# Kernel tuning notes

Hardware: AMD Instinct MI355X
Metric: run time of the kernel (lower is better)

Reference implementation:

```python
import jax, jax.numpy as jnp
import numpy as np

N_NODES = 50000
N_EDGES = 640000
IN_C, HID_C, OUT_C = 64, 128, 64


def _glorot(key, fan_in, fan_out):
    lim = float(np.sqrt(6.0 / (fan_in + fan_out)))
    return jax.random.uniform(key, (fan_in, fan_out), jnp.float32, -lim, lim)


def setup_inputs() -> dict:
    key = jax.random.key(0)
    ks = jax.random.split(key, 16)
    x = jax.random.normal(ks[0], (N_NODES, IN_C), jnp.float32)
    edge_index = jax.random.randint(ks[1], (2, N_EDGES), 0, N_NODES, jnp.int64)
    # SAGEConv params: out = mean_aggr(x_j) @ Wl + x @ Wr + b
    dims = [(IN_C, HID_C), (HID_C, HID_C), (HID_C, OUT_C)]
    params = {}
    for i, (fi, fo) in enumerate(dims):
        params[f"Wl{i}"] = _glorot(ks[2 + 3 * i], fi, fo)
        params[f"Wr{i}"] = _glorot(ks[3 + 3 * i], fi, fo)
        params[f"b{i}"] = jnp.zeros((fo,), jnp.float32)
    # classifier: Linear(64,32) -> ReLU -> Linear(32,1) -> Sigmoid (dropout off in eval)
    params["Wc1"] = _glorot(ks[11], OUT_C, 32)
    params["bc1"] = jnp.zeros((32,), jnp.float32)
    params["Wc2"] = _glorot(ks[12], 32, 1)
    params["bc2"] = jnp.zeros((1,), jnp.float32)
    return {"x": x, "edge_index": edge_index, **params}


def _sage_conv(x, src, dst, Wl, Wr, b):
    # gather neighbor (source) features along edges, mean-aggregate at target
    msgs = x[src]                                                    # [E, C]
    agg = jax.ops.segment_sum(msgs, dst, num_segments=N_NODES)      # [N, C]
    deg = jax.ops.segment_sum(jnp.ones((src.shape[0], 1), x.dtype), dst,
                              num_segments=N_NODES)                 # [N, 1]
    agg = agg / jnp.maximum(deg, 1.0)
    return agg @ Wl + x @ Wr + b


def reference(x, edge_index, Wl0, Wr0, b0, Wl1, Wr1, b1, Wl2, Wr2, b2,
              Wc1, bc1, Wc2, bc2):
    src, dst = edge_index[0], edge_index[1]
    h = jax.nn.relu(_sage_conv(x, src, dst, Wl0, Wr0, b0))
    h = jax.nn.relu(_sage_conv(h, src, dst, Wl1, Wr1, b1))
    h = _sage_conv(h, src, dst, Wl2, Wr2, b2)                       # [N, 64]
    h = jax.nn.relu(h @ Wc1 + bc1)                                  # [N, 32]
    return jax.nn.sigmoid(h @ Wc2 + bc2)                            # [N, 1]
```

## Files before the change

### kernel.cpp

```cpp
#include <hip/hip_runtime.h>
#include <hip/hip_cooperative_groups.h>
#include <math.h>

namespace cg = cooperative_groups;

#define NN 50000
#define NE 640000
#define CAP 64

typedef short short8 __attribute__((ext_vector_type(8)));
typedef float f32x4  __attribute__((ext_vector_type(4)));

__device__ __forceinline__ unsigned bfr(float f) {
    unsigned u = __float_as_uint(f);
    return (u + 0x7FFFu + ((u >> 16) & 1u)) >> 16;
}
__device__ __forceinline__ unsigned pk2(float a, float b) { return bfr(a) | (bfr(b) << 16); }
__device__ __forceinline__ float bflo(unsigned u) { return __uint_as_float(u << 16); }
__device__ __forceinline__ float bfhi(unsigned u) { return __uint_as_float(u & 0xFFFF0000u); }

__device__ __forceinline__ void packOne(const float* Wl, const float* Wr,
                                        unsigned short* wp, int idx,
                                        int CIN, int COUT) {
    int k = idx / COUT, n = idx % COUT;
    float v = (k < CIN) ? Wl[k * COUT + n] : Wr[(k - CIN) * COUT + n];
    int kt = k >> 5, quad = (k >> 3) & 3, j = k & 7;
    int nt = n >> 4, l16 = n & 15;
    int NT = COUT / 16;
    wp[(((kt * NT + nt) * 64) + quad * 16 + l16) * 8 + j] = (unsigned short)bfr(v);
}

template <int CIN, int COUT, bool RELU, bool CLS>
__device__ __forceinline__ void
fused_layer(const unsigned* __restrict__ Fu, const unsigned short* __restrict__ Fs,
            const int* __restrict__ nbr, const int* __restrict__ cnt,
            const unsigned short* __restrict__ Wpack, const float* __restrict__ bias,
            unsigned short* __restrict__ outp,
            const unsigned short* __restrict__ WpackC, const float* __restrict__ bc1,
            const float* __restrict__ Wc2, const float* __restrict__ bc2,
            float* __restrict__ outf,
            short* __restrict__ lds, int blk, int gstride, int t) {
    constexpr int RU = CIN / 2;
    constexpr int PC = RU / 16;
    constexpr int RS = CIN + 8;
    constexpr int RSu = RS / 2;
    constexpr int KT = (2 * CIN) / 32;
    constexpr int NT = COUT / 16;
    constexpr int CS = 136;
    const int NTILE = (NN + 127) / 128;

    const int g = t >> 4, lg = t & 15;
    const int wave = t >> 6, lane = t & 63;
    const int quad = lane >> 4, l16 = lane & 15;

    for (int tile = blk; tile < NTILE; tile += gstride) {
#pragma unroll 1
        for (int i = 0; i < 8; ++i) {
            const int rloc = g * 8 + i;
            const int gw = tile * 128 + rloc;
            unsigned* lrow = (unsigned*)lds + rloc * RSu + lg * PC;
            if (gw < NN) {
                const int deg = cnt[gw];
                const int m = (deg < CAP) ? deg : CAP;
                float a[2 * PC] = {};
                for (int base = 0; base < m; base += 16) {
                    int idx = NN;
                    if (base + lg < m) idx = nbr[gw * CAP + base + lg];
#pragma unroll
                    for (int j = 0; j < 16; ++j) {
                        const int n = __shfl(idx, j, 16);
                        if (PC == 2) {
                            const uint2 u = *(const uint2*)(Fu + (size_t)n * RU + lg * 2);
                            a[0] += bflo(u.x); a[1] += bfhi(u.x);
                            a[2] += bflo(u.y); a[3] += bfhi(u.y);
                        } else {
                            const uint4 u = *(const uint4*)(Fu + (size_t)n * RU + lg * 4);
                            a[0] += bflo(u.x); a[1] += bfhi(u.x);
                            a[2] += bflo(u.y); a[3] += bfhi(u.y);
                            a[4] += bflo(u.z); a[5] += bfhi(u.z);
                            a[6] += bflo(u.w); a[7] += bfhi(u.w);
                        }
                    }
                }
                const float di = 1.0f / (float)((deg > 1) ? deg : 1);
                if (PC == 2)
                    *(uint2*)lrow = make_uint2(pk2(a[0] * di, a[1] * di),
                                               pk2(a[2] * di, a[3] * di));
                else
                    *(uint4*)lrow = make_uint4(pk2(a[0] * di, a[1] * di),
                                               pk2(a[2] * di, a[3] * di),
                                               pk2(a[4] * di, a[5] * di),
                                               pk2(a[6] * di, a[7] * di));
            } else {
                if (PC == 2) *(uint2*)lrow = make_uint2(0u, 0u);
                else         *(uint4*)lrow = make_uint4(0u, 0u, 0u, 0u);
            }
        }
        __syncthreads();

        const int rbase = tile * 128 + wave * 32;
        int r0 = rbase + l16;      if (r0 >= NN) r0 = NN - 1;
        int r1 = rbase + 16 + l16; if (r1 >= NN) r1 = NN - 1;
        const int rl0 = wave * 32 + l16, rl1 = rl0 + 16;

        f32x4 acc[2][NT] = {};
#pragma unroll
        for (int kt = 0; kt < KT; ++kt) {
            short8 a0, a1;
            if (kt < KT / 2) {
                a0 = *(const short8*)(lds + rl0 * RS + kt * 32 + quad * 8);
                a1 = *(const short8*)(lds + rl1 * RS + kt * 32 + quad * 8);
            } else {
                a0 = *(const short8*)(Fs + (size_t)r0 * CIN + (kt * 32 - CIN) + quad * 8);
                a1 = *(const short8*)(Fs + (size_t)r1 * CIN + (kt * 32 - CIN) + quad * 8);
            }
#pragma unroll
            for (int nt = 0; nt < NT; ++nt) {
                const short8 bfrag = *(const short8*)(Wpack + (size_t)((kt * NT + nt) * 64 + lane) * 8);
                acc[0][nt] = __builtin_amdgcn_mfma_f32_16x16x32_bf16(a0, bfrag, acc[0][nt], 0, 0, 0);
                acc[1][nt] = __builtin_amdgcn_mfma_f32_16x16x32_bf16(a1, bfrag, acc[1][nt], 0, 0, 0);
            }
        }
        __syncthreads();

        if constexpr (!CLS) {
#pragma unroll
            for (int nt = 0; nt < NT; ++nt) {
                const float bb = bias[nt * 16 + l16];
#pragma unroll
                for (int s = 0; s < 2; ++s)
#pragma unroll
                    for (int rg = 0; rg < 4; ++rg) {
                        const int rloc = wave * 32 + s * 16 + quad * 4 + rg;
                        float v = acc[s][nt][rg] + bb;
                        if (RELU) v = fmaxf(v, 0.f);
                        lds[rloc * CS + nt * 16 + l16] = (short)(unsigned short)bfr(v);
                    }
            }
            __syncthreads();
            constexpr int CH = COUT / 8;
            for (int idx = t; idx < 128 * CH; idx += 256) {
                const int row = idx / CH, c8 = idx % CH;
                const int gr = tile * 128 + row;
                if (gr < NN)
                    *(uint4*)(outp + (size_t)gr * COUT + c8 * 8) =
                        *(const uint4*)(lds + row * CS + c8 * 8);
            }
            __syncthreads();
        } else {
            constexpr int HS = 72;
#pragma unroll
            for (int nt = 0; nt < NT; ++nt) {
                const float bb = bias[nt * 16 + l16];
#pragma unroll
                for (int s = 0; s < 2; ++s)
#pragma unroll
                    for (int rg = 0; rg < 4; ++rg) {
                        const int rloc = wave * 32 + s * 16 + quad * 4 + rg;
                        lds[rloc * HS + nt * 16 + l16] =
                            (short)(unsigned short)bfr(acc[s][nt][rg] + bb);
                    }
            }
            __syncthreads();

            f32x4 sacc[2][2] = {};
#pragma unroll
            for (int s = 0; s < 2; ++s) {
                const int rloc = wave * 32 + s * 16 + l16;
#pragma unroll
                for (int kt2 = 0; kt2 < 2; ++kt2) {
                    const short8 af = *(const short8*)(lds + rloc * HS + kt2 * 32 + quad * 8);
#pragma unroll
                    for (int nt2 = 0; nt2 < 2; ++nt2) {
                        const short8 bf = *(const short8*)(WpackC + (size_t)((kt2 * 2 + nt2) * 64 + lane) * 8);
                        sacc[s][nt2] = __builtin_amdgcn_mfma_f32_16x16x32_bf16(af, bf, sacc[s][nt2], 0, 0, 0);
                    }
                }
            }

            const float b1a = bc1[l16], b1b = bc1[16 + l16];
            const float w2a = Wc2[l16], w2b = Wc2[16 + l16];
            const float b2v = bc2[0];
#pragma unroll
            for (int s = 0; s < 2; ++s)
#pragma unroll
                for (int rg = 0; rg < 4; ++rg) {
                    float p = fmaxf(sacc[s][0][rg] + b1a, 0.f) * w2a +
                              fmaxf(sacc[s][1][rg] + b1b, 0.f) * w2b;
#pragma unroll
                    for (int off = 1; off < 16; off <<= 1) p += __shfl_xor(p, off);
                    if (l16 == 0) {
                        const int row = tile * 128 + wave * 32 + s * 16 + quad * 4 + rg;
                        if (row < NN) outf[row] = 1.0f / (1.0f + expf(-(p + b2v)));
                    }
                }
            __syncthreads();
        }
    }
}

__global__ __launch_bounds__(256) void
k_all(const int* __restrict__ src, const int* __restrict__ dst,
      const float* __restrict__ x,
      const float* Wl0, const float* Wr0, const float* b0,
      const float* Wl1, const float* Wr1, const float* b1,
      const float* Wl2, const float* Wr2, const float* b2,
      const float* Wc1, const float* bc1, const float* Wc2, const float* bc2,
      int* cnt, int* nbr, unsigned short* xb,
      unsigned short* wp0, unsigned short* wp1, unsigned short* wp2,
      unsigned short* wpc,
      unsigned short* aggb, unsigned short* h0b, unsigned short* h1b,
      float* out) {
    cg::grid_group grid = cg::this_grid();
    (void)aggb;

    __shared__ __align__(16) short lds[128 * 136];

    const int t = threadIdx.x, b = blockIdx.x;
    const int nthr = gridDim.x * 256;
    const int gt = b * 256 + t;

    for (int e = gt; e < NE; e += nthr) {
        int d = dst[e];
        int p = atomicAdd(&cnt[d], 1);
        if (p < CAP) nbr[d * CAP + p] = src[e];
    }
    for (int i = gt; i < NN * 16; i += nthr) {
        float4 v = ((const float4*)x)[i];
        ((uint2*)xb)[i] = make_uint2(pk2(v.x, v.y), pk2(v.z, v.w));
    }
    if (gt < 32) ((unsigned*)xb)[(size_t)NN * 32 + gt] = 0u;
    else if (gt < 96) ((unsigned*)h0b)[(size_t)NN * 64 + (gt - 32)] = 0u;
    else if (gt < 160) ((unsigned*)h1b)[(size_t)NN * 64 + (gt - 96)] = 0u;
    for (int i = gt; i < 67584; i += nthr) {
        if (i < 16384) packOne(Wl0, Wr0, wp0, i, 64, 128);
        else if (i < 49152) packOne(Wl1, Wr1, wp1, i - 16384, 128, 128);
        else if (i < 65536) packOne(Wl2, Wr2, wp2, i - 49152, 128, 64);
        else packOne(Wc1, Wc1, wpc, i - 65536, 64, 32);
    }
    grid.sync();

    fused_layer<64, 128, true, false>((const unsigned*)xb, xb, nbr, cnt, wp0, b0, h0b,
                                      nullptr, nullptr, nullptr, nullptr, nullptr,
                                      lds, b, gridDim.x, t);
    grid.sync();

    fused_layer<128, 128, true, false>((const unsigned*)h0b, h0b, nbr, cnt, wp1, b1, h1b,
                                       nullptr, nullptr, nullptr, nullptr, nullptr,
                                       lds, b, gridDim.x, t);
    grid.sync();

    fused_layer<128, 64, false, true>((const unsigned*)h1b, h1b, nbr, cnt, wp2, b2, nullptr,
                                      wpc, bc1, Wc2, bc2, out,
                                      lds, b, gridDim.x, t);
}

template <int LOGC>
__device__ __forceinline__ void
agg_phase(const unsigned* __restrict__ xu, const int* __restrict__ nbr,
          const int* __restrict__ cnt, unsigned* __restrict__ aggu,
          int gid, int ngroups, int l16) {
    constexpr int RU = 1 << (LOGC - 1);
    constexpr int PC = RU / 16;

    for (int gw = gid; gw < NN; gw += ngroups) {
        const int deg = cnt[gw];
        const int m = (deg < CAP) ? deg : CAP;

        float a[2 * PC] = {};

        for (int base = 0; base < m; base += 16) {
            int idx = NN;
            if (base + l16 < m) idx = nbr[gw * CAP + base + l16];
#pragma unroll
            for (int j = 0; j < 16; ++j) {
                const int n = __shfl(idx, j, 16);
                if (PC == 2) {
                    const uint2 u = *(const uint2*)(xu + (size_t)n * RU + l16 * 2);
                    a[0] += bflo(u.x); a[1] += bfhi(u.x);
                    a[2] += bflo(u.y); a[3] += bfhi(u.y);
                } else {
                    const uint4 u = *(const uint4*)(xu + (size_t)n * RU + l16 * 4);
                    a[0] += bflo(u.x); a[1] += bfhi(u.x);
                    a[2] += bflo(u.y); a[3] += bfhi(u.y);
                    a[4] += bflo(u.z); a[5] += bfhi(u.z);
                    a[6] += bflo(u.w); a[7] += bfhi(u.w);
                }
            }
        }

        const float di = 1.0f / (float)((deg > 1) ? deg : 1);
        if (PC == 2) {
            uint2 o = make_uint2(pk2(a[0] * di, a[1] * di), pk2(a[2] * di, a[3] * di));
            *(uint2*)(aggu + (size_t)gw * RU + l16 * 2) = o;
        } else {
            uint4 o = make_uint4(pk2(a[0] * di, a[1] * di), pk2(a[2] * di, a[3] * di),
                                 pk2(a[4] * di, a[5] * di), pk2(a[6] * di, a[7] * di));
            *(uint4*)(aggu + (size_t)gw * RU + l16 * 4) = o;
        }
    }
}

template <int CIN, int COUT, bool RELU>
__device__ __forceinline__ void
mfma_phase(const unsigned short* __restrict__ Agg, const unsigned short* __restrict__ X,
           const unsigned short* __restrict__ Wpack, const float* __restrict__ bias,
           unsigned short* __restrict__ outp, int blk, int gstride, int wave, int lane) {
    constexpr int KT = (2 * CIN) / 32;
    constexpr int NT = COUT / 16;
    const int quad = lane >> 4, l16 = lane & 15;
    const int NTILE = (NN + 127) / 128;

    for (int tile = blk; tile < NTILE; tile += gstride) {
        const int row_base = tile * 128 + wave * 32;
        int r0 = row_base + l16;      if (r0 >= NN) r0 = NN - 1;
        int r1 = row_base + 16 + l16; if (r1 >= NN) r1 = NN - 1;

        f32x4 acc[2][NT] = {};

        for (int kt = 0; kt < KT; ++kt) {
            const unsigned short* P = (kt < KT / 2) ? Agg : X;
            const int kb = (kt < KT / 2) ? kt * 32 : kt * 32 - CIN;
            const short8 a0 = *(const short8*)(P + (size_t)r0 * CIN + kb + quad * 8);
            const short8 a1 = *(const short8*)(P + (size_t)r1 * CIN + kb + quad * 8);
#pragma unroll
            for (int nt = 0; nt < NT; ++nt) {
                const short8 bfrag = *(const short8*)(Wpack + (size_t)((kt * NT + nt) * 64 + lane) * 8);
                acc[0][nt] = __builtin_amdgcn_mfma_f32_16x16x32_bf16(a0, bfrag, acc[0][nt], 0, 0, 0);
                acc[1][nt] = __builtin_amdgcn_mfma_f32_16x16x32_bf16(a1, bfrag, acc[1][nt], 0, 0, 0);
            }
        }

#pragma unroll
        for (int nt = 0; nt < NT; ++nt) {
            const int col = nt * 16 + l16;
            const float bb = bias[col];
#pragma unroll
            for (int s = 0; s < 2; ++s) {
#pragma unroll
                for (int rg = 0; rg < 4; ++rg) {
                    int row = row_base + s * 16 + quad * 4 + rg;
                    if (row < NN) {
                        float v = acc[s][nt][rg] + bb;
                        if (RELU) v = fmaxf(v, 0.f);
                        outp[(size_t)row * COUT + col] = (unsigned short)bfr(v);
                    }
                }
            }
        }
    }
}

__global__ __launch_bounds__(256) void
k_prep(const int* __restrict__ src, const int* __restrict__ dst,
       int* __restrict__ cnt, int* __restrict__ nbr,
       const float* __restrict__ x, unsigned* __restrict__ xb,
       const float* Wl0, const float* Wr0, const float* Wl1, const float* Wr1,
       const float* Wl2, const float* Wr2, const float* Wc1,
       unsigned short* wp0, unsigned short* wp1, unsigned short* wp2,
       unsigned short* wpc, unsigned short* h0b, unsigned short* h1b) {
    const int b = blockIdx.x, t = threadIdx.x;
    if (b < 2500) {
        int e = b * 256 + t;
        if (e < NE) {
            int d = dst[e];
            int p = atomicAdd(&cnt[d], 1);
            if (p < CAP) nbr[d * CAP + p] = src[e];
        }
        if (b == 0) {
            if (t < 32) xb[(size_t)NN * 32 + t] = 0u;
            else if (t < 96) ((unsigned*)h0b)[(size_t)NN * 64 + (t - 32)] = 0u;
            else if (t < 160) ((unsigned*)h1b)[(size_t)NN * 64 + (t - 96)] = 0u;
        }
    } else if (b < 5625) {
        int i = (b - 2500) * 256 + t;
        if (i < NN * 16) {
            float4 v = ((const float4*)x)[i];
            ((uint2*)xb)[i] = make_uint2(pk2(v.x, v.y), pk2(v.z, v.w));
        }
    } else {
        int idx = (b - 5625) * 256 + t;
        if (idx < 16384) packOne(Wl0, Wr0, wp0, idx, 64, 128);
        else if (idx < 49152) packOne(Wl1, Wr1, wp1, idx - 16384, 128, 128);
        else if (idx < 65536) packOne(Wl2, Wr2, wp2, idx - 49152, 128, 64);
        else if (idx < 67584) packOne(Wc1, Wc1, wpc, idx - 65536, 64, 32);
    }
}

template <int LOGC>
__global__ __launch_bounds__(256) void
k_aggregate(const unsigned* __restrict__ xu, const int* __restrict__ nbr,
            const int* __restrict__ cnt, unsigned* __restrict__ aggu, int N) {
    const int gid = (blockIdx.x * 256 + threadIdx.x) >> 4;
    if (gid >= N) return;
    agg_phase<LOGC>(xu, nbr, cnt, aggu, gid, 1 << 30, threadIdx.x & 15);
}

template <int CIN, int COUT, bool RELU>
__global__ __launch_bounds__(256) void
k_mfma(const unsigned short* __restrict__ Agg, const unsigned short* __restrict__ X,
       const unsigned short* __restrict__ Wpack, const float* __restrict__ bias,
       unsigned short* __restrict__ outp, int N) {
    mfma_phase<CIN, COUT, RELU>(Agg, X, Wpack, bias, outp,
                                blockIdx.x, 1 << 30, threadIdx.x >> 6, threadIdx.x & 63);
}

__global__ __launch_bounds__(256) void
k_mfma_cls(const unsigned short* __restrict__ Agg, const unsigned short* __restrict__ X,
           const unsigned short* __restrict__ Wpack, const unsigned short* __restrict__ WpackC,
           const float* __restrict__ bias, const float* __restrict__ bc1,
           const float* __restrict__ Wc2, const float* __restrict__ bc2,
           float* __restrict__ out, int N) {
    constexpr int CIN = 128, NT = 4, KT = 8;

    __shared__ __align__(16) short Hs[8 * 16 * 64];

    const int t = threadIdx.x;
    const int wave = t >> 6, lane = t & 63;
    const int quad = lane >> 4, l16 = lane & 15;

    const int row_base = blockIdx.x * 128 + wave * 32;
    int r0 = row_base + l16;      if (r0 >= N) r0 = N - 1;
    int r1 = row_base + 16 + l16; if (r1 >= N) r1 = N - 1;

    f32x4 acc[2][NT] = {};

    for (int kt = 0; kt < KT; ++kt) {
        const unsigned short* P = (kt < KT / 2) ? Agg : X;
        const int kb = (kt < KT / 2) ? kt * 32 : kt * 32 - CIN;
        const short8 a0 = *(const short8*)(P + (size_t)r0 * CIN + kb + quad * 8);
        const short8 a1 = *(const short8*)(P + (size_t)r1 * CIN + kb + quad * 8);
#pragma unroll
        for (int nt = 0; nt < NT; ++nt) {
            const short8 bfrag = *(const short8*)(Wpack + (size_t)((kt * NT + nt) * 64 + lane) * 8);
            acc[0][nt] = __builtin_amdgcn_mfma_f32_16x16x32_bf16(a0, bfrag, acc[0][nt], 0, 0, 0);
            acc[1][nt] = __builtin_amdgcn_mfma_f32_16x16x32_bf16(a1, bfrag, acc[1][nt], 0, 0, 0);
        }
    }

#pragma unroll
    for (int nt = 0; nt < NT; ++nt) {
        const float bb = bias[nt * 16 + l16];
#pragma unroll
        for (int s = 0; s < 2; ++s)
#pragma unroll
            for (int rg = 0; rg < 4; ++rg)
                Hs[(wave * 2 + s) * 1024 + (quad * 4 + rg) * 64 + nt * 16 + l16] =
                    (unsigned short)bfr(acc[s][nt][rg] + bb);
    }
    __syncthreads();

    f32x4 sacc[2][2] = {};
#pragma unroll
    for (int s = 0; s < 2; ++s)
#pragma unroll
        for (int kt2 = 0; kt2 < 2; ++kt2) {
            const short8 af = *(const short8*)&Hs[(wave * 2 + s) * 1024 + l16 * 64 +
                                                  kt2 * 32 + quad * 8];
#pragma unroll
            for (int nt2 = 0; nt2 < 2; ++nt2) {
                const short8 bf = *(const short8*)(WpackC + (size_t)((kt2 * 2 + nt2) * 64 + lane) * 8);
                sacc[s][nt2] = __builtin_amdgcn_mfma_f32_16x16x32_bf16(af, bf, sacc[s][nt2], 0, 0, 0);
            }
        }

    const float b1a = bc1[l16], b1b = bc1[16 + l16];
    const float w2a = Wc2[l16], w2b = Wc2[16 + l16];
    const float b2v = bc2[0];
#pragma unroll
    for (int s = 0; s < 2; ++s)
#pragma unroll
        for (int rg = 0; rg < 4; ++rg) {
            float p = fmaxf(sacc[s][0][rg] + b1a, 0.f) * w2a +
                      fmaxf(sacc[s][1][rg] + b1b, 0.f) * w2b;
#pragma unroll
            for (int off = 1; off < 16; off <<= 1) p += __shfl_xor(p, off);
            if (l16 == 0) {
                int row = row_base + s * 16 + quad * 4 + rg;
                if (row < N) out[row] = 1.0f / (1.0f + expf(-(p + b2v)));
            }
        }
}

extern "C" void kernel_launch(void* const* d_in, const int* in_sizes, int n_in,
                              void* d_out, int out_size, void* d_ws, size_t ws_size,
                              hipStream_t stream) {
    const float* x   = (const float*)d_in[0];
    const int*   ei  = (const int*)d_in[1];
    const int*   src = ei;
    const int*   dst = ei + NE;
    const float* Wl0 = (const float*)d_in[2];
    const float* Wr0 = (const float*)d_in[3];
    const float* b0  = (const float*)d_in[4];
    const float* Wl1 = (const float*)d_in[5];
    const float* Wr1 = (const float*)d_in[6];
    const float* b1  = (const float*)d_in[7];
    const float* Wl2 = (const float*)d_in[8];
    const float* Wr2 = (const float*)d_in[9];
    const float* b2  = (const float*)d_in[10];
    const float* Wc1 = (const float*)d_in[11];
    const float* bc1 = (const float*)d_in[12];
    const float* Wc2 = (const float*)d_in[13];
    const float* bc2 = (const float*)d_in[14];
    float* out = (float*)d_out;

    char*  ws   = (char*)d_ws;
    int*   cnt  = (int*)(ws);
    unsigned short* wp0 = (unsigned short*)(ws + (size_t)256 * 1024);
    unsigned short* wp1 = (unsigned short*)(ws + (size_t)352 * 1024);
    unsigned short* wp2 = (unsigned short*)(ws + (size_t)448 * 1024);
    unsigned short* wpc = (unsigned short*)(ws + (size_t)512 * 1024);
    int*   nbr  = (int*)(ws + (size_t)1 * (1 << 20));
    unsigned short* xb   = (unsigned short*)(ws + (size_t)16 * (1 << 20));
    unsigned short* aggb = (unsigned short*)(ws + (size_t)24 * (1 << 20));
    unsigned short* h0b  = (unsigned short*)(ws + (size_t)40 * (1 << 20));
    unsigned short* h1b  = (unsigned short*)(ws + (size_t)56 * (1 << 20));

    hipMemsetAsync(cnt, 0, (size_t)NN * sizeof(int), stream);

    bool coop_ok = false;
    int maxBpc = 0, ncu = 0, dev = 0;
    hipGetDevice(&dev);
    hipDeviceGetAttribute(&ncu, hipDeviceAttributeMultiprocessorCount, dev);
    hipError_t qerr = hipOccupancyMaxActiveBlocksPerMultiprocessor(
        &maxBpc, (const void*)k_all, 256, 0);
    if (qerr == hipSuccess && maxBpc > 0 && ncu > 0) {
        int grid = maxBpc * ncu;
        if (grid > 2048) grid = 2048;
        const int* srcp = src; const int* dstp = dst;
        void* args[] = {
            (void*)&srcp, (void*)&dstp, (void*)&x,
            (void*)&Wl0, (void*)&Wr0, (void*)&b0,
            (void*)&Wl1, (void*)&Wr1, (void*)&b1,
            (void*)&Wl2, (void*)&Wr2, (void*)&b2,
            (void*)&Wc1, (void*)&bc1, (void*)&Wc2, (void*)&bc2,
            (void*)&cnt, (void*)&nbr, (void*)&xb,
            (void*)&wp0, (void*)&wp1, (void*)&wp2, (void*)&wpc,
            (void*)&aggb, (void*)&h0b, (void*)&h1b,
            (void*)&out
        };
        hipError_t lerr = hipLaunchCooperativeKernel((const void*)k_all, dim3(grid),
                                                     dim3(256), args, 0, stream);
        if (lerr == hipSuccess) coop_ok = true;
        else (void)hipGetLastError();
    } else {
        (void)hipGetLastError();
    }

    if (!coop_ok) {
        const int B = 256;
        const int AGG_GRID = (NN * 16 + 255) / 256;
        const int MFMA_GRID = (NN + 127) / 128;

        k_prep<<<5889, B, 0, stream>>>(src, dst, cnt, nbr, x, (unsigned*)xb,
                                       Wl0, Wr0, Wl1, Wr1, Wl2, Wr2, Wc1,
                                       wp0, wp1, wp2, wpc, h0b, h1b);

        k_aggregate<6><<<AGG_GRID, B, 0, stream>>>((const unsigned*)xb, nbr, cnt,
                                                   (unsigned*)aggb, NN);
        k_mfma<64, 128, true><<<MFMA_GRID, B, 0, stream>>>(aggb, xb, wp0, b0, h0b, NN);

        k_aggregate<7><<<AGG_GRID, B, 0, stream>>>((const unsigned*)h0b, nbr, cnt,
                                                   (unsigned*)aggb, NN);
        k_mfma<128, 128, true><<<MFMA_GRID, B, 0, stream>>>(aggb, h0b, wp1, b1, h1b, NN);

        k_aggregate<7><<<AGG_GRID, B, 0, stream>>>((const unsigned*)h1b, nbr, cnt,
                                                   (unsigned*)aggb, NN);
        k_mfma_cls<<<MFMA_GRID, B, 0, stream>>>(aggb, h1b, wp2, wpc, b2, bc1, Wc2, bc2,
                                                out, NN);
    }
}
```

Measured before the change: 234.3 us.

## Replace cooperative persistent kernel with per-layer fused kernel launches

Drops the single cooperative kernel that used grid-wide syncs between phases. It is replaced by a prep kernel followed by three launches, one per layer, each fusing aggregation with the MFMA matmul and using one block per 128-row tile. Kernel boundaries now provide the inter-layer synchronization, and grid occupancy is no longer capped by the resident-block limit. The cost is extra launch overhead and less flexible load balancing across tiles.

```diff
diff --git a/kernel.cpp b/kernel.cpp
--- a/kernel.cpp
+++ b/kernel.cpp
@@ -1,8 +1,5 @@
 #include <hip/hip_runtime.h>
-#include <hip/hip_cooperative_groups.h>
 #include <math.h>
-
-namespace cg = cooperative_groups;
 
 #define NN 50000
 #define NE 640000
@@ -39,7 +36,7 @@
             const unsigned short* __restrict__ WpackC, const float* __restrict__ bc1,
             const float* __restrict__ Wc2, const float* __restrict__ bc2,
             float* __restrict__ outf,
-            short* __restrict__ lds, int blk, int gstride, int t) {
+            short* __restrict__ lds, int tile, int t) {
     constexpr int RU = CIN / 2;
     constexpr int PC = RU / 16;
     constexpr int RS = CIN + 8;
@@ -47,308 +44,166 @@
     constexpr int KT = (2 * CIN) / 32;
     constexpr int NT = COUT / 16;
     constexpr int CS = 136;
-    const int NTILE = (NN + 127) / 128;
 
     const int g = t >> 4, lg = t & 15;
     const int wave = t >> 6, lane = t & 63;
     const int quad = lane >> 4, l16 = lane & 15;
 
-    for (int tile = blk; tile < NTILE; tile += gstride) {
 #pragma unroll 1
-        for (int i = 0; i < 8; ++i) {
-            const int rloc = g * 8 + i;
-            const int gw = tile * 128 + rloc;
-            unsigned* lrow = (unsigned*)lds + rloc * RSu + lg * PC;
-            if (gw < NN) {
-                const int deg = cnt[gw];
-                const int m = (deg < CAP) ? deg : CAP;
-                float a[2 * PC] = {};
-                for (int base = 0; base < m; base += 16) {
-                    int idx = NN;
-                    if (base + lg < m) idx = nbr[gw * CAP + base + lg];
-#pragma unroll
-                    for (int j = 0; j < 16; ++j) {
-                        const int n = __shfl(idx, j, 16);
-                        if (PC == 2) {
-                            const uint2 u = *(const uint2*)(Fu + (size_t)n * RU + lg * 2);
-                            a[0] += bflo(u.x); a[1] += bfhi(u.x);
-                            a[2] += bflo(u.y); a[3] += bfhi(u.y);
-                        } else {
-                            const uint4 u = *(const uint4*)(Fu + (size_t)n * RU + lg * 4);
-                            a[0] += bflo(u.x); a[1] += bfhi(u.x);
-                            a[2] += bflo(u.y); a[3] += bfhi(u.y);
-                            a[4] += bflo(u.z); a[5] += bfhi(u.z);
-                            a[6] += bflo(u.w); a[7] += bfhi(u.w);
-                        }
+    for (int i = 0; i < 8; ++i) {
+        const int rloc = g * 8 + i;
+        const int gw = tile * 128 + rloc;
+        unsigned* lrow = (unsigned*)lds + rloc * RSu + lg * PC;
+        if (gw < NN) {
+            const int deg = cnt[gw];
+            const int m = (deg < CAP) ? deg : CAP;
+            float a[2 * PC] = {};
+            for (int base = 0; base < m; base += 16) {
+                int idx = NN;
+                if (base + lg < m) idx = nbr[gw * CAP + base + lg];
+#pragma unroll
+                for (int j = 0; j < 16; ++j) {
+                    const int n = __shfl(idx, j, 16);
+                    if (PC == 2) {
+                        const uint2 u = *(const uint2*)(Fu + (size_t)n * RU + lg * 2);
+                        a[0] += bflo(u.x); a[1] += bfhi(u.x);
+                        a[2] += bflo(u.y); a[3] += bfhi(u.y);
+                    } else {
+                        const uint4 u = *(const uint4*)(Fu + (size_t)n * RU + lg * 4);
+                        a[0] += bflo(u.x); a[1] += bfhi(u.x);
+                        a[2] += bflo(u.y); a[3] += bfhi(u.y);
+                        a[4] += bflo(u.z); a[5] += bfhi(u.z);
+                        a[6] += bflo(u.w); a[7] += bfhi(u.w);
                     }
                 }
-                const float di = 1.0f / (float)((deg > 1) ? deg : 1);
-                if (PC == 2)
-                    *(uint2*)lrow = make_uint2(pk2(a[0] * di, a[1] * di),
-                                               pk2(a[2] * di, a[3] * di));
-                else
-                    *(uint4*)lrow = make_uint4(pk2(a[0] * di, a[1] * di),
-                                               pk2(a[2] * di, a[3] * di),
-                                               pk2(a[4] * di, a[5] * di),
-                                               pk2(a[6] * di, a[7] * di));
-            } else {
-                if (PC == 2) *(uint2*)lrow = make_uint2(0u, 0u);
-                else         *(uint4*)lrow = make_uint4(0u, 0u, 0u, 0u);
             }
+            const float di = 1.0f / (float)((deg > 1) ? deg : 1);
+            if (PC == 2)
+                *(uint2*)lrow = make_uint2(pk2(a[0] * di, a[1] * di),
+                                           pk2(a[2] * di, a[3] * di));
+            else
+                *(uint4*)lrow = make_uint4(pk2(a[0] * di, a[1] * di),
+                                           pk2(a[2] * di, a[3] * di),
+                                           pk2(a[4] * di, a[5] * di),
+                                           pk2(a[6] * di, a[7] * di));
+        } else {
+            if (PC == 2) *(uint2*)lrow = make_uint2(0u, 0u);
+            else         *(uint4*)lrow = make_uint4(0u, 0u, 0u, 0u);
+        }
+    }
+    __syncthreads();
+
+    const int rbase = tile * 128 + wave * 32;
+    int r0 = rbase + l16;      if (r0 >= NN) r0 = NN - 1;
+    int r1 = rbase + 16 + l16; if (r1 >= NN) r1 = NN - 1;
+    const int rl0 = wave * 32 + l16, rl1 = rl0 + 16;
+
+    f32x4 acc[2][NT] = {};
+#pragma unroll
+    for (int kt = 0; kt < KT; ++kt) {
+        short8 a0, a1;
+        if (kt < KT / 2) {
+            a0 = *(const short8*)(lds + rl0 * RS + kt * 32 + quad * 8);
+            a1 = *(const short8*)(lds + rl1 * RS + kt * 32 + quad * 8);
+        } else {
+            a0 = *(const short8*)(Fs + (size_t)r0 * CIN + (kt * 32 - CIN) + quad * 8);
+            a1 = *(const short8*)(Fs + (size_t)r1 * CIN + (kt * 32 - CIN) + quad * 8);
+        }
+#pragma unroll
+        for (int nt = 0; nt < NT; ++nt) {
+            const short8 bfrag = *(const short8*)(Wpack + (size_t)((kt * NT + nt) * 64 + lane) * 8);
+            acc[0][nt] = __builtin_amdgcn_mfma_f32_16x16x32_bf16(a0, bfrag, acc[0][nt], 0, 0, 0);
+            acc[1][nt] = __builtin_amdgcn_mfma_f32_16x16x32_bf16(a1, bfrag, acc[1][nt], 0, 0, 0);
+        }
+    }
+    __syncthreads();
+
+    if constexpr (!CLS) {
+#pragma unroll
+        for (int nt = 0; nt < NT; ++nt) {
+            const float bb = bias[nt * 16 + l16];
+#pragma unroll
+            for (int s = 0; s < 2; ++s)
+#pragma unroll
+                for (int rg = 0; rg < 4; ++rg) {
+                    const int rloc = wave * 32 + s * 16 + quad * 4 + rg;
+                    float v = acc[s][nt][rg] + bb;
+                    if (RELU) v = fmaxf(v, 0.f);
+                    lds[rloc * CS + nt * 16 + l16] = (short)(unsigned short)bfr(v);
+                }
         }
         __syncthreads();
-
-        const int rbase = tile * 128 + wave * 32;
-        int r0 = rbase + l16;      if (r0 >= NN) r0 = NN - 1;
-        int r1 = rbase + 16 + l16; if (r1 >= NN) r1 = NN - 1;
-        const int rl0 = wave * 32 + l16, rl1 = rl0 + 16;
-
-        f32x4 acc[2][NT] = {};
-#pragma unroll
-        for (int kt = 0; kt < KT; ++kt) {
-            short8 a0, a1;
-            if (kt < KT / 2) {
-                a0 = *(const short8*)(lds + rl0 * RS + kt * 32 + quad * 8);
-                a1 = *(const short8*)(lds + rl1 * RS + kt * 32 + quad * 8);
-            } else {
-                a0 = *(const short8*)(Fs + (size_t)r0 * CIN + (kt * 32 - CIN) + quad * 8);
-                a1 = *(const short8*)(Fs + (size_t)r1 * CIN + (kt * 32 - CIN) + quad * 8);
+        constexpr int CH = COUT / 8;
+        for (int idx = t; idx < 128 * CH; idx += 256) {
+            const int row = idx / CH, c8 = idx % CH;
+            const int gr = tile * 128 + row;
+            if (gr < NN)
+                *(uint4*)(outp + (size_t)gr * COUT + c8 * 8) =
+                    *(const uint4*)(lds + row * CS + c8 * 8);
+        }
+    } else {
+        constexpr int HS = 72;
+#pragma unroll
+        for (int nt = 0; nt < NT; ++nt) {
+            const float bb = bias[nt * 16 + l16];
+#pragma unroll
+            for (int s = 0; s < 2; ++s)
+#pragma unroll
+                for (int rg = 0; rg < 4; ++rg) {
+                    const int rloc = wave * 32 + s * 16 + quad * 4 + rg;
+                    lds[rloc * HS + nt * 16 + l16] =
+                        (short)(unsigned short)bfr(acc[s][nt][rg] + bb);
+                }
+        }
+        __syncthreads();
+
+        f32x4 sacc[2][2] = {};
+#pragma unroll
+        for (int s = 0; s < 2; ++s) {
+            const int rloc = wave * 32 + s * 16 + l16;
+#pragma unroll
+            for (int kt2 = 0; kt2 < 2; ++kt2) {
+                const short8 af = *(const short8*)(lds + rloc * HS + kt2 * 32 + quad * 8);
+#pragma unroll
+                for (int nt2 = 0; nt2 < 2; ++nt2) {
+                    const short8 bf = *(const short8*)(WpackC + (size_t)((kt2 * 2 + nt2) * 64 + lane) * 8);
+                    sacc[s][nt2] = __builtin_amdgcn_mfma_f32_16x16x32_bf16(af, bf, sacc[s][nt2], 0, 0, 0);
+                }
             }
-#pragma unroll
-            for (int nt = 0; nt < NT; ++nt) {
-                const short8 bfrag = *(const short8*)(Wpack + (size_t)((kt * NT + nt) * 64 + lane) * 8);
-                acc[0][nt] = __builtin_amdgcn_mfma_f32_16x16x32_bf16(a0, bfrag, acc[0][nt], 0, 0, 0);
-                acc[1][nt] = __builtin_amdgcn_mfma_f32_16x16x32_bf16(a1, bfrag, acc[1][nt], 0, 0, 0);
+        }
+
+        const float b1a = bc1[l16], b1b = bc1[16 + l16];
+        const float w2a = Wc2[l16], w2b = Wc2[16 + l16];
+        const float b2v = bc2[0];
+#pragma unroll
+        for (int s = 0; s < 2; ++s)
+#pragma unroll
+            for (int rg = 0; rg < 4; ++rg) {
+                float p = fmaxf(sacc[s][0][rg] + b1a, 0.f) * w2a +
+                          fmaxf(sacc[s][1][rg] + b1b, 0.f) * w2b;
+#pragma unroll
+                for (int off = 1; off < 16; off <<= 1) p += __shfl_xor(p, off);
+                if (l16 == 0) {
+                    const int row = tile * 128 + wave * 32 + s * 16 + quad * 4 + rg;
+                    if (row < NN) outf[row] = 1.0f / (1.0f + expf(-(p + b2v)));
+                }
             }
-        }
-        __syncthreads();
-
-        if constexpr (!CLS) {
-#pragma unroll
-            for (int nt = 0; nt < NT; ++nt) {
-                const float bb = bias[nt * 16 + l16];
-#pragma unroll
-                for (int s = 0; s < 2; ++s)
-#pragma unroll
-                    for (int rg = 0; rg < 4; ++rg) {
-                        const int rloc = wave * 32 + s * 16 + quad * 4 + rg;
-                        float v = acc[s][nt][rg] + bb;
-                        if (RELU) v = fmaxf(v, 0.f);
-                        lds[rloc * CS + nt * 16 + l16] = (short)(unsigned short)bfr(v);
-                    }
-            }
-            __syncthreads();
-            constexpr int CH = COUT / 8;
-            for (int idx = t; idx < 128 * CH; idx += 256) {
-                const int row = idx / CH, c8 = idx % CH;
-                const int gr = tile * 128 + row;
-                if (gr < NN)
-                    *(uint4*)(outp + (size_t)gr * COUT + c8 * 8) =
-                        *(const uint4*)(lds + row * CS + c8 * 8);
-            }
-            __syncthreads();
-        } else {
-            constexpr int HS = 72;
-#pragma unroll
-            for (int nt = 0; nt < NT; ++nt) {
-                const float bb = bias[nt * 16 + l16];
-#pragma unroll
-                for (int s = 0; s < 2; ++s)
-#pragma unroll
-                    for (int rg = 0; rg < 4; ++rg) {
-                        const int rloc = wave * 32 + s * 16 + quad * 4 + rg;
-                        lds[rloc * HS + nt * 16 + l16] =
-                            (short)(unsigned short)bfr(acc[s][nt][rg] + bb);
-                    }
-            }
-            __syncthreads();
-
-            f32x4 sacc[2][2] = {};
-#pragma unroll
-            for (int s = 0; s < 2; ++s) {
-                const int rloc = wave * 32 + s * 16 + l16;
-#pragma unroll
-                for (int kt2 = 0; kt2 < 2; ++kt2) {
-                    const short8 af = *(const short8*)(lds + rloc * HS + kt2 * 32 + quad * 8);
-#pragma unroll
-                    for (int nt2 = 0; nt2 < 2; ++nt2) {
-                        const short8 bf = *(const short8*)(WpackC + (size_t)((kt2 * 2 + nt2) * 64 + lane) * 8);
-                        sacc[s][nt2] = __builtin_amdgcn_mfma_f32_16x16x32_bf16(af, bf, sacc[s][nt2], 0, 0, 0);
-                    }
-                }
-            }
-
-            const float b1a = bc1[l16], b1b = bc1[16 + l16];
-            const float w2a = Wc2[l16], w2b = Wc2[16 + l16];
-            const float b2v = bc2[0];
-#pragma unroll
-            for (int s = 0; s < 2; ++s)
-#pragma unroll
-                for (int rg = 0; rg < 4; ++rg) {
-                    float p = fmaxf(sacc[s][0][rg] + b1a, 0.f) * w2a +
-                              fmaxf(sacc[s][1][rg] + b1b, 0.f) * w2b;
-#pragma unroll
-                    for (int off = 1; off < 16; off <<= 1) p += __shfl_xor(p, off);
-                    if (l16 == 0) {
-                        const int row = tile * 128 + wave * 32 + s * 16 + quad * 4 + rg;
-                        if (row < NN) outf[row] = 1.0f / (1.0f + expf(-(p + b2v)));
-                    }
-                }
-            __syncthreads();
-        }
-    }
-}
-
+    }
+}
+
+template <int CIN, int COUT, bool RELU, bool CLS>
 __global__ __launch_bounds__(256) void
-k_all(const int* __restrict__ src, const int* __restrict__ dst,
-      const float* __restrict__ x,
-      const float* Wl0, const float* Wr0, const float* b0,
-      const float* Wl1, const float* Wr1, const float* b1,
-      const float* Wl2, const float* Wr2, const float* b2,
-      const float* Wc1, const float* bc1, const float* Wc2, const float* bc2,
-      int* cnt, int* nbr, unsigned short* xb,
-      unsigned short* wp0, unsigned short* wp1, unsigned short* wp2,
-      unsigned short* wpc,
-      unsigned short* aggb, unsigned short* h0b, unsigned short* h1b,
-      float* out) {
-    cg::grid_group grid = cg::this_grid();
-    (void)aggb;
-
+k_fused(const unsigned* __restrict__ Fu, const unsigned short* __restrict__ Fs,
+        const int* __restrict__ nbr, const int* __restrict__ cnt,
+        const unsigned short* __restrict__ Wpack, const float* __restrict__ bias,
+        unsigned short* __restrict__ outp,
+        const unsigned short* __restrict__ WpackC, const float* __restrict__ bc1,
+        const float* __restrict__ Wc2, const float* __restrict__ bc2,
+        float* __restrict__ outf) {
     __shared__ __align__(16) short lds[128 * 136];
-
-    const int t = threadIdx.x, b = blockIdx.x;
-    const int nthr = gridDim.x * 256;
-    const int gt = b * 256 + t;
-
-    for (int e = gt; e < NE; e += nthr) {
-        int d = dst[e];
-        int p = atomicAdd(&cnt[d], 1);
-        if (p < CAP) nbr[d * CAP + p] = src[e];
-    }
-    for (int i = gt; i < NN * 16; i += nthr) {
-        float4 v = ((const float4*)x)[i];
-        ((uint2*)xb)[i] = make_uint2(pk2(v.x, v.y), pk2(v.z, v.w));
-    }
-    if (gt < 32) ((unsigned*)xb)[(size_t)NN * 32 + gt] = 0u;
-    else if (gt < 96) ((unsigned*)h0b)[(size_t)NN * 64 + (gt - 32)] = 0u;
-    else if (gt < 160) ((unsigned*)h1b)[(size_t)NN * 64 + (gt - 96)] = 0u;
-    for (int i = gt; i < 67584; i += nthr) {
-        if (i < 16384) packOne(Wl0, Wr0, wp0, i, 64, 128);
-        else if (i < 49152) packOne(Wl1, Wr1, wp1, i - 16384, 128, 128);
-        else if (i < 65536) packOne(Wl2, Wr2, wp2, i - 49152, 128, 64);
-        else packOne(Wc1, Wc1, wpc, i - 65536, 64, 32);
-    }
-    grid.sync();
-
-    fused_layer<64, 128, true, false>((const unsigned*)xb, xb, nbr, cnt, wp0, b0, h0b,
-                                      nullptr, nullptr, nullptr, nullptr, nullptr,
-                                      lds, b, gridDim.x, t);
-    grid.sync();
-
-    fused_layer<128, 128, true, false>((const unsigned*)h0b, h0b, nbr, cnt, wp1, b1, h1b,
-                                       nullptr, nullptr, nullptr, nullptr, nullptr,
-                                       lds, b, gridDim.x, t);
-    grid.sync();
-
-    fused_layer<128, 64, false, true>((const unsigned*)h1b, h1b, nbr, cnt, wp2, b2, nullptr,
-                                      wpc, bc1, Wc2, bc2, out,
-                                      lds, b, gridDim.x, t);
-}
-
-template <int LOGC>
-__device__ __forceinline__ void
-agg_phase(const unsigned* __restrict__ xu, const int* __restrict__ nbr,
-          const int* __restrict__ cnt, unsigned* __restrict__ aggu,
-          int gid, int ngroups, int l16) {
-    constexpr int RU = 1 << (LOGC - 1);
-    constexpr int PC = RU / 16;
-
-    for (int gw = gid; gw < NN; gw += ngroups) {
-        const int deg = cnt[gw];
-        const int m = (deg < CAP) ? deg : CAP;
-
-        float a[2 * PC] = {};
-
-        for (int base = 0; base < m; base += 16) {
-            int idx = NN;
-            if (base + l16 < m) idx = nbr[gw * CAP + base + l16];
-#pragma unroll
-            for (int j = 0; j < 16; ++j) {
-                const int n = __shfl(idx, j, 16);
-                if (PC == 2) {
-                    const uint2 u = *(const uint2*)(xu + (size_t)n * RU + l16 * 2);
-                    a[0] += bflo(u.x); a[1] += bfhi(u.x);
-                    a[2] += bflo(u.y); a[3] += bfhi(u.y);
-                } else {
-                    const uint4 u = *(const uint4*)(xu + (size_t)n * RU + l16 * 4);
-                    a[0] += bflo(u.x); a[1] += bfhi(u.x);
-                    a[2] += bflo(u.y); a[3] += bfhi(u.y);
-                    a[4] += bflo(u.z); a[5] += bfhi(u.z);
-                    a[6] += bflo(u.w); a[7] += bfhi(u.w);
-                }
-            }
-        }
-
-        const float di = 1.0f / (float)((deg > 1) ? deg : 1);
-        if (PC == 2) {
-            uint2 o = make_uint2(pk2(a[0] * di, a[1] * di), pk2(a[2] * di, a[3] * di));
-            *(uint2*)(aggu + (size_t)gw * RU + l16 * 2) = o;
-        } else {
-            uint4 o = make_uint4(pk2(a[0] * di, a[1] * di), pk2(a[2] * di, a[3] * di),
-                                 pk2(a[4] * di, a[5] * di), pk2(a[6] * di, a[7] * di));
-            *(uint4*)(aggu + (size_t)gw * RU + l16 * 4) = o;
-        }
-    }
-}
-
-template <int CIN, int COUT, bool RELU>
-__device__ __forceinline__ void
-mfma_phase(const unsigned short* __restrict__ Agg, const unsigned short* __restrict__ X,
-           const unsigned short* __restrict__ Wpack, const float* __restrict__ bias,
-           unsigned short* __restrict__ outp, int blk, int gstride, int wave, int lane) {
-    constexpr int KT = (2 * CIN) / 32;
-    constexpr int NT = COUT / 16;
-    const int quad = lane >> 4, l16 = lane & 15;
-    const int NTILE = (NN + 127) / 128;
-
-    for (int tile = blk; tile < NTILE; tile += gstride) {
-        const int row_base = tile * 128 + wave * 32;
-        int r0 = row_base + l16;      if (r0 >= NN) r0 = NN - 1;
-        int r1 = row_base + 16 + l16; if (r1 >= NN) r1 = NN - 1;
-
-        f32x4 acc[2][NT] = {};
-
-        for (int kt = 0; kt < KT; ++kt) {
-            const unsigned short* P = (kt < KT / 2) ? Agg : X;
-            const int kb = (kt < KT / 2) ? kt * 32 : kt * 32 - CIN;
-            const short8 a0 = *(const short8*)(P + (size_t)r0 * CIN + kb + quad * 8);
-            const short8 a1 = *(const short8*)(P + (size_t)r1 * CIN + kb + quad * 8);
-#pragma unroll
-            for (int nt = 0; nt < NT; ++nt) {
-                const short8 bfrag = *(const short8*)(Wpack + (size_t)((kt * NT + nt) * 64 + lane) * 8);
-                acc[0][nt] = __builtin_amdgcn_mfma_f32_16x16x32_bf16(a0, bfrag, acc[0][nt], 0, 0, 0);
-                acc[1][nt] = __builtin_amdgcn_mfma_f32_16x16x32_bf16(a1, bfrag, acc[1][nt], 0, 0, 0);
-            }
-        }
-
-#pragma unroll
-        for (int nt = 0; nt < NT; ++nt) {
-            const int col = nt * 16 + l16;
-            const float bb = bias[col];
-#pragma unroll
-            for (int s = 0; s < 2; ++s) {
-#pragma unroll
-                for (int rg = 0; rg < 4; ++rg) {
-                    int row = row_base + s * 16 + quad * 4 + rg;
-                    if (row < NN) {
-                        float v = acc[s][nt][rg] + bb;
-                        if (RELU) v = fmaxf(v, 0.f);
-                        outp[(size_t)row * COUT + col] = (unsigned short)bfr(v);
-                    }
-                }
-            }
-        }
-    }
+    fused_layer<CIN, COUT, RELU, CLS>(Fu, Fs, nbr, cnt, Wpack, bias, outp,
+                                      WpackC, bc1, Wc2, bc2, outf,
+                                      lds, blockIdx.x, threadIdx.x);
 }
 
 __global__ __launch_bounds__(256) void
@@ -385,101 +240,6 @@
         else if (idx < 65536) packOne(Wl2, Wr2, wp2, idx - 49152, 128, 64);
         else if (idx < 67584) packOne(Wc1, Wc1, wpc, idx - 65536, 64, 32);
     }
-}
-
-template <int LOGC>
-__global__ __launch_bounds__(256) void
-k_aggregate(const unsigned* __restrict__ xu, const int* __restrict__ nbr,
-            const int* __restrict__ cnt, unsigned* __restrict__ aggu, int N) {
-    const int gid = (blockIdx.x * 256 + threadIdx.x) >> 4;
-    if (gid >= N) return;
-    agg_phase<LOGC>(xu, nbr, cnt, aggu, gid, 1 << 30, threadIdx.x & 15);
-}
-
-template <int CIN, int COUT, bool RELU>
-__global__ __launch_bounds__(256) void
-k_mfma(const unsigned short* __restrict__ Agg, const unsigned short* __restrict__ X,
-       const unsigned short* __restrict__ Wpack, const float* __restrict__ bias,
-       unsigned short* __restrict__ outp, int N) {
-    mfma_phase<CIN, COUT, RELU>(Agg, X, Wpack, bias, outp,
-                                blockIdx.x, 1 << 30, threadIdx.x >> 6, threadIdx.x & 63);
-}
-
-__global__ __launch_bounds__(256) void
-k_mfma_cls(const unsigned short* __restrict__ Agg, const unsigned short* __restrict__ X,
-           const unsigned short* __restrict__ Wpack, const unsigned short* __restrict__ WpackC,
-           const float* __restrict__ bias, const float* __restrict__ bc1,
-           const float* __restrict__ Wc2, const float* __restrict__ bc2,
-           float* __restrict__ out, int N) {
-    constexpr int CIN = 128, NT = 4, KT = 8;
-
-    __shared__ __align__(16) short Hs[8 * 16 * 64];
-
-    const int t = threadIdx.x;
-    const int wave = t >> 6, lane = t & 63;
-    const int quad = lane >> 4, l16 = lane & 15;
-
-    const int row_base = blockIdx.x * 128 + wave * 32;
-    int r0 = row_base + l16;      if (r0 >= N) r0 = N - 1;
-    int r1 = row_base + 16 + l16; if (r1 >= N) r1 = N - 1;
-
-    f32x4 acc[2][NT] = {};
-
-    for (int kt = 0; kt < KT; ++kt) {
-        const unsigned short* P = (kt < KT / 2) ? Agg : X;
-        const int kb = (kt < KT / 2) ? kt * 32 : kt * 32 - CIN;
-        const short8 a0 = *(const short8*)(P + (size_t)r0 * CIN + kb + quad * 8);
-        const short8 a1 = *(const short8*)(P + (size_t)r1 * CIN + kb + quad * 8);
-#pragma unroll
-        for (int nt = 0; nt < NT; ++nt) {
-            const short8 bfrag = *(const short8*)(Wpack + (size_t)((kt * NT + nt) * 64 + lane) * 8);
-            acc[0][nt] = __builtin_amdgcn_mfma_f32_16x16x32_bf16(a0, bfrag, acc[0][nt], 0, 0, 0);
-            acc[1][nt] = __builtin_amdgcn_mfma_f32_16x16x32_bf16(a1, bfrag, acc[1][nt], 0, 0, 0);
-        }
-    }
-
-#pragma unroll
-    for (int nt = 0; nt < NT; ++nt) {
-        const float bb = bias[nt * 16 + l16];
-#pragma unroll
-        for (int s = 0; s < 2; ++s)
-#pragma unroll
-            for (int rg = 0; rg < 4; ++rg)
-                Hs[(wave * 2 + s) * 1024 + (quad * 4 + rg) * 64 + nt * 16 + l16] =
-                    (unsigned short)bfr(acc[s][nt][rg] + bb);
-    }
-    __syncthreads();
-
-    f32x4 sacc[2][2] = {};
-#pragma unroll
-    for (int s = 0; s < 2; ++s)
-#pragma unroll
-        for (int kt2 = 0; kt2 < 2; ++kt2) {
-            const short8 af = *(const short8*)&Hs[(wave * 2 + s) * 1024 + l16 * 64 +
-                                                  kt2 * 32 + quad * 8];
-#pragma unroll
-            for (int nt2 = 0; nt2 < 2; ++nt2) {
-                const short8 bf = *(const short8*)(WpackC + (size_t)((kt2 * 2 + nt2) * 64 + lane) * 8);
-                sacc[s][nt2] = __builtin_amdgcn_mfma_f32_16x16x32_bf16(af, bf, sacc[s][nt2], 0, 0, 0);
-            }
-        }
-
-    const float b1a = bc1[l16], b1b = bc1[16 + l16];
-    const float w2a = Wc2[l16], w2b = Wc2[16 + l16];
-    const float b2v = bc2[0];
-#pragma unroll
-    for (int s = 0; s < 2; ++s)
-#pragma unroll
-        for (int rg = 0; rg < 4; ++rg) {
-            float p = fmaxf(sacc[s][0][rg] + b1a, 0.f) * w2a +
-                      fmaxf(sacc[s][1][rg] + b1b, 0.f) * w2b;
-#pragma unroll
-            for (int off = 1; off < 16; off <<= 1) p += __shfl_xor(p, off);
-            if (l16 == 0) {
-                int row = row_base + s * 16 + quad * 4 + rg;
-                if (row < N) out[row] = 1.0f / (1.0f + expf(-(p + b2v)));
-            }
-        }
 }
 
 extern "C" void kernel_launch(void* const* d_in, const int* in_sizes, int n_in,
@@ -512,61 +272,27 @@
     unsigned short* wpc = (unsigned short*)(ws + (size_t)512 * 1024);
     int*   nbr  = (int*)(ws + (size_t)1 * (1 << 20));
     unsigned short* xb   = (unsigned short*)(ws + (size_t)16 * (1 << 20));
-    unsigned short* aggb = (unsigned short*)(ws + (size_t)24 * (1 << 20));
     unsigned short* h0b  = (unsigned short*)(ws + (size_t)40 * (1 << 20));
     unsigned short* h1b  = (unsigned short*)(ws + (size_t)56 * (1 << 20));
 
     hipMemsetAsync(cnt, 0, (size_t)NN * sizeof(int), stream);
 
-    bool coop_ok = false;
-    int maxBpc = 0, ncu = 0, dev = 0;
-    hipGetDevice(&dev);
-    hipDeviceGetAttribute(&ncu, hipDeviceAttributeMultiprocessorCount, dev);
-    hipError_t qerr = hipOccupancyMaxActiveBlocksPerMultiprocessor(
-        &maxBpc, (const void*)k_all, 256, 0);
-    if (qerr == hipSuccess && maxBpc > 0 && ncu > 0) {
-        int grid = maxBpc * ncu;
-        if (grid > 2048) grid = 2048;
-        const int* srcp = src; const int* dstp = dst;
-        void* args[] = {
-            (void*)&srcp, (void*)&dstp, (void*)&x,
-            (void*)&Wl0, (void*)&Wr0, (void*)&b0,
-            (void*)&Wl1, (void*)&Wr1, (void*)&b1,
-            (void*)&Wl2, (void*)&Wr2, (void*)&b2,
-            (void*)&Wc1, (void*)&bc1, (void*)&Wc2, (void*)&bc2,
-            (void*)&cnt, (void*)&nbr, (void*)&xb,
-            (void*)&wp0, (void*)&wp1, (void*)&wp2, (void*)&wpc,
-            (void*)&aggb, (void*)&h0b, (void*)&h1b,
-            (void*)&out
-        };
-        hipError_t lerr = hipLaunchCooperativeKernel((const void*)k_all, dim3(grid),
-                                                     dim3(256), args, 0, stream);
-        if (lerr == hipSuccess) coop_ok = true;
-        else (void)hipGetLastError();
-    } else {
-        (void)hipGetLastError();
-    }
-
-    if (!coop_ok) {
-        const int B = 256;
-        const int AGG_GRID = (NN * 16 + 255) / 256;
-        const int MFMA_GRID = (NN + 127) / 128;
-
-        k_prep<<<5889, B, 0, stream>>>(src, dst, cnt, nbr, x, (unsigned*)xb,
-                                       Wl0, Wr0, Wl1, Wr1, Wl2, Wr2, Wc1,
-                                       wp0, wp1, wp2, wpc, h0b, h1b);
-
-        k_aggregate<6><<<AGG_GRID, B, 0, stream>>>((const unsigned*)xb, nbr, cnt,
-                                                   (unsigned*)aggb, NN);
-        k_mfma<64, 128, true><<<MFMA_GRID, B, 0, stream>>>(aggb, xb, wp0, b0, h0b, NN);
-
-        k_aggregate<7><<<AGG_GRID, B, 0, stream>>>((const unsigned*)h0b, nbr, cnt,
-                                                   (unsigned*)aggb, NN);
-        k_mfma<128, 128, true><<<MFMA_GRID, B, 0, stream>>>(aggb, h0b, wp1, b1, h1b, NN);
-
-        k_aggregate<7><<<AGG_GRID, B, 0, stream>>>((const unsigned*)h1b, nbr, cnt,
-                                                   (unsigned*)aggb, NN);
-        k_mfma_cls<<<MFMA_GRID, B, 0, stream>>>(aggb, h1b, wp2, wpc, b2, bc1, Wc2, bc2,
-                                                out, NN);
-    }
-}
+    const int B = 256;
+    const int NTILE = (NN + 127) / 128;
+
+    k_prep<<<5889, B, 0, stream>>>(src, dst, cnt, nbr, x, (unsigned*)xb,
+                                   Wl0, Wr0, Wl1, Wr1, Wl2, Wr2, Wc1,
+                                   wp0, wp1, wp2, wpc, h0b, h1b);
+
+    k_fused<64, 128, true, false><<<NTILE, B, 0, stream>>>(
+        (const unsigned*)xb, xb, nbr, cnt, wp0, b0, h0b,
+        nullptr, nullptr, nullptr, nullptr, nullptr);
+
+    k_fused<128, 128, true, false><<<NTILE, B, 0, stream>>>(
+        (const unsigned*)h0b, h0b, nbr, cnt, wp1, b1, h1b,
+        nullptr, nullptr, nullptr, nullptr, nullptr);
+
+    k_fused<128, 64, false, true><<<NTILE, B, 0, stream>>>(
+        (const unsigned*)h1b, h1b, nbr, cnt, wp2, b2, nullptr,
+        wpc, bc1, Wc2, bc2, out);
+}
```

After: 235.9 us. Within noise of the previous version (+0.7%).
